# Kernel tuning notes

Hardware: AMD Instinct MI355X
Metric: run time of the kernel (lower is better)

## Reference

```python
import jax, jax.numpy as jnp
import numpy as np

B, T = 4, 1024
MF, EF, DM, DF, HN, L = 256, 512, 512, 2048, 8, 6
HD = DM // HN  # 64
D = MF + EF // 2  # 512, feature dim of x / mask_in


def prelu(x, a):
    return jnp.where(x >= 0, x, a * x)


def layer_norm(x, g, b, eps=1e-5):
    m = x.mean(-1, keepdims=True)
    v = ((x - m) ** 2).mean(-1, keepdims=True)
    return (x - m) / jnp.sqrt(v + eps) * g + b


def skew_relative(QE):
    # QE: (B, H, N, 2N-1) -> (B, H, N, N) via the pad/reshape/slice skew trick
    b, h, n = QE.shape[0], QE.shape[1], QE.shape[2]
    q = jnp.pad(QE, ((0, 0), (0, 0), (0, 0), (0, 1))).reshape(b, h, -1)
    q = jnp.pad(q, ((0, 0), (0, 0), (0, n - 1))).reshape(b, h, n + 1, 2 * n - 1)
    return q[:, :, :n, -n:]


def setup_inputs() -> dict:
    key = jax.random.key(0)
    ks = iter(jax.random.split(key, 80))
    rn = lambda shape, s: jax.random.normal(next(ks), shape, dtype=jnp.float32) * s
    si = lambda fan: fan ** -0.5
    inp = {}
    inp['x'] = rn((B, T, D), 1.0)
    inp['mask_in'] = (jax.random.uniform(next(ks), (B, T, D)) > 0.2).astype(jnp.float32)
    inp['p_kf'] = rn((B, T, 2), 1.0)
    inp['enc_w1'] = rn((2 * D, DM), si(2 * D)); inp['enc_b1'] = jnp.zeros((DM,)); inp['enc_a1'] = 0.25 * jnp.ones((1,))
    inp['enc_w2'] = rn((DM, DM), si(DM)); inp['enc_b2'] = jnp.zeros((DM,)); inp['enc_a2'] = 0.25 * jnp.ones((1,))
    inp['kf_w1'] = rn((2, DM), si(2)); inp['kf_b1'] = jnp.zeros((DM,)); inp['kf_a'] = 0.25 * jnp.ones((1,))
    inp['kf_w2'] = rn((DM, DM), si(DM)); inp['kf_b2'] = jnp.zeros((DM,))
    inp['rel_w1'] = rn((1, DM), 1.0); inp['rel_b1'] = jnp.zeros((DM,)); inp['rel_a'] = 0.25 * jnp.ones((1,))
    inp['rel_w2'] = rn((DM, HD), si(DM)); inp['rel_b2'] = jnp.zeros((HD,))
    inp['ln_g'] = jnp.ones((DM,)); inp['ln_b'] = jnp.zeros((DM,))
    inp['attn_wq'] = rn((L, DM, DM), si(DM))
    inp['attn_wk'] = rn((L, DM, DM), si(DM))
    inp['attn_wv'] = rn((L, DM, DM), si(DM))
    inp['attn_wo'] = rn((L, DM, DM), si(DM)); inp['attn_wob'] = jnp.zeros((L, DM))
    inp['ffn_w1'] = rn((L, DM, DF), si(DM)); inp['ffn_b1'] = jnp.zeros((L, DF)); inp['ffn_a'] = 0.25 * jnp.ones((L, 1))
    inp['ffn_w2'] = rn((L, DF, DM), si(DF)); inp['ffn_b2'] = jnp.zeros((L, DM))
    inp['dec_w1'] = rn((DM, DM), si(DM)); inp['dec_b1'] = jnp.zeros((DM,)); inp['dec_a'] = 0.25 * jnp.ones((1,))
    inp['dec_w2'] = rn((DM, MF), si(DM)); inp['dec_b2'] = jnp.zeros((MF,))
    return inp


def reference(x, mask_in, p_kf, enc_w1, enc_b1, enc_a1, enc_w2, enc_b2, enc_a2,
              kf_w1, kf_b1, kf_a, kf_w2, kf_b2, rel_w1, rel_b1, rel_a, rel_w2, rel_b2,
              ln_g, ln_b, attn_wq, attn_wk, attn_wv, attn_wo, attn_wob,
              ffn_w1, ffn_b1, ffn_a, ffn_w2, ffn_b2, dec_w1, dec_b1, dec_a, dec_w2, dec_b2):
    b, t, _ = x.shape
    # keyframe positional encoding + context encoder
    pe_kf = prelu(p_kf @ kf_w1 + kf_b1, kf_a) @ kf_w2 + kf_b2
    h = prelu(jnp.concatenate([x, mask_in], -1) @ enc_w1 + enc_b1, enc_a1)
    h = prelu(h @ enc_w2 + enc_b2, enc_a2) + pe_kf
    # relative position embedding table E: (2T-1, HD)
    rel = jnp.arange(-t + 1, t, dtype=jnp.float32)[:, None]
    E = prelu(rel @ rel_w1 + rel_b1, rel_a) @ rel_w2 + rel_b2
    # attention mask from mask_in (broadcast over heads/queries)
    valid = mask_in.sum(-1) > 0
    mask_att = jnp.where(valid, 0.0, -1e9)[:, None, None, :]  # (B,1,1,T)
    scale = HD ** -0.5
    nl = attn_wq.shape[0]
    for i in range(nl):
        hn = layer_norm(h, ln_g, ln_b)
        Q = (hn @ attn_wq[i]).reshape(b, t, HN, HD).transpose(0, 2, 1, 3)
        K = (hn @ attn_wk[i]).reshape(b, t, HN, HD).transpose(0, 2, 1, 3)
        V = (hn @ attn_wv[i]).reshape(b, t, HN, HD).transpose(0, 2, 1, 3)
        att = jnp.einsum('bhqd,bhkd->bhqk', Q, K)
        att = att + skew_relative(jnp.einsum('bhqd,rd->bhqr', Q, E))
        att = jax.nn.softmax(att * scale + mask_att, axis=-1)
        o = jnp.einsum('bhqk,bhkd->bhqd', att, V).transpose(0, 2, 1, 3).reshape(b, t, HN * HD)
        h = h + o @ attn_wo[i] + attn_wob[i]
        hn = layer_norm(h, ln_g, ln_b)
        h = h + prelu(hn @ ffn_w1[i] + ffn_b1[i], ffn_a[i]) @ ffn_w2[i] + ffn_b2[i]
    return prelu(h @ dec_w1 + dec_b1, dec_a) @ dec_w2 + dec_b2
```

## Files before the change

### kernel.cpp

```cpp
#include <hip/hip_runtime.h>
#include <cstddef>

#define BB 4
#define TT 1024
#define DMODEL 512
#define DFF 2048
#define NHEAD 8
#define HDIM 64
#define NTOK (BB*TT)
#define NLAYER 6
#define MFOUT 256
#define LDS_STRIDE 72
#define SPLITK 4

typedef __attribute__((ext_vector_type(8))) _Float16 f16x8;
typedef __attribute__((ext_vector_type(8))) short bf16x8;
typedef __attribute__((ext_vector_type(4))) float f32x4;
#define MFMAH(a,b,c) __builtin_amdgcn_mfma_f32_16x16x32_f16(a,b,c,0,0,0)
#define MFMAB(a,b,c) __builtin_amdgcn_mfma_f32_16x16x32_bf16(a,b,c,0,0,0)

union F16U { _Float16 h; unsigned short u; };

__device__ __forceinline__ unsigned f2bf(float f) {
    union { float f; unsigned u; } v; v.f = f;
    return (v.u + 0x7FFFu + ((v.u >> 16) & 1u)) >> 16;
}
__device__ __forceinline__ float bf2f(unsigned h) {
    union { unsigned u; float f; } v; v.u = h << 16;
    return v.f;
}
__device__ __forceinline__ unsigned short f16u(float v) {
    F16U t; t.h = (_Float16)v; return t.u;
}

#define MODE_F32  0
#define MODE_BF   1
#define MODE_QKV  5

__global__ __launch_bounds__(256)
void wcvt(const float* __restrict__ W, unsigned short* __restrict__ Wh,
          unsigned short* __restrict__ Wl, int N, int K)
{
    __shared__ unsigned short Hs[64][LDS_STRIDE];
    __shared__ unsigned short Ls[64][LDS_STRIDE];
    const int tid = threadIdx.x;
    const int n0 = blockIdx.x * 64, k0 = blockIdx.y * 64;
    #pragma unroll
    for (int i = 0; i < 4; i++) {
        const int idx = tid + i * 256;
        const int r = idx >> 4, c4 = (idx & 15) * 4;
        const float4 v = *(const float4*)&W[(size_t)(k0 + r) * N + n0 + c4];
        const float va[4] = {v.x, v.y, v.z, v.w};
        #pragma unroll
        for (int j = 0; j < 4; j++) {
            const unsigned h = f2bf(va[j]);
            Hs[c4 + j][r] = (unsigned short)h;
            Ls[c4 + j][r] = (unsigned short)f2bf(va[j] - bf2f(h));
        }
    }
    __syncthreads();
    #pragma unroll
    for (int i = 0; i < 2; i++) {
        const int idx = tid + i * 256;
        const int r = idx >> 3, c8 = (idx & 7) * 8;
        *(uint4*)&Wh[(size_t)(n0 + r) * K + k0 + c8] = *(const uint4*)&Hs[r][c8];
        *(uint4*)&Wl[(size_t)(n0 + r) * K + k0 + c8] = *(const uint4*)&Ls[r][c8];
    }
}

__global__ __launch_bounds__(256)
void gemm_l(const unsigned short* __restrict__ Ah, const unsigned short* __restrict__ Al,
            const unsigned short* __restrict__ Wh, const unsigned short* __restrict__ Wl,
            const float* __restrict__ bias, const float* __restrict__ alpha,
            const float* __restrict__ res, float* __restrict__ outf,
            unsigned short* __restrict__ o1, unsigned short* __restrict__ o2,
            unsigned short* __restrict__ o3, unsigned short* __restrict__ o4,
            unsigned short* __restrict__ o5, int N, int K, int mode)
{
    __shared__ __align__(16) unsigned short Ahs[64*LDS_STRIDE];
    __shared__ __align__(16) unsigned short Als[64*LDS_STRIDE];
    __shared__ __align__(16) unsigned short Whs[64*LDS_STRIDE];
    __shared__ __align__(16) unsigned short Wls[64*LDS_STRIDE];
    const int tid = threadIdx.x;
    const int lane = tid & 63, w = tid >> 6;
    const int wm = w >> 1, wn = w & 1;
    const int quad = lane >> 4, c = lane & 15;
    const int m0 = blockIdx.y * 64, n0 = blockIdx.x * 64;
    const int sr = tid >> 2, sc = (tid & 3) * 16;

    f32x4 acc[2][2];
    #pragma unroll
    for (int mi = 0; mi < 2; mi++)
        #pragma unroll
        for (int ni = 0; ni < 2; ni++) { acc[mi][ni][0]=0.f; acc[mi][ni][1]=0.f; acc[mi][ni][2]=0.f; acc[mi][ni][3]=0.f; }

    for (int k0 = 0; k0 < K; k0 += 64) {
        const size_t ga = (size_t)(m0 + sr) * K + k0 + sc;
        const size_t gb = (size_t)(n0 + sr) * K + k0 + sc;
        const int ls = sr * LDS_STRIDE + sc;
        *(uint4*)&Ahs[ls]     = *(const uint4*)&Ah[ga];
        *(uint4*)&Ahs[ls + 8] = *(const uint4*)&Ah[ga + 8];
        *(uint4*)&Als[ls]     = *(const uint4*)&Al[ga];
        *(uint4*)&Als[ls + 8] = *(const uint4*)&Al[ga + 8];
        *(uint4*)&Whs[ls]     = *(const uint4*)&Wh[gb];
        *(uint4*)&Whs[ls + 8] = *(const uint4*)&Wh[gb + 8];
        *(uint4*)&Wls[ls]     = *(const uint4*)&Wl[gb];
        *(uint4*)&Wls[ls + 8] = *(const uint4*)&Wl[gb + 8];
        __syncthreads();
        #pragma unroll
        for (int s = 0; s < 2; s++) {
            const int ao = (wm * 32 + c) * LDS_STRIDE + s * 32 + quad * 8;
            const int bo = (wn * 32 + c) * LDS_STRIDE + s * 32 + quad * 8;
            const bf16x8 ah0 = *(const bf16x8*)&Ahs[ao];
            const bf16x8 ah1 = *(const bf16x8*)&Ahs[ao + 16 * LDS_STRIDE];
            const bf16x8 al0 = *(const bf16x8*)&Als[ao];
            const bf16x8 al1 = *(const bf16x8*)&Als[ao + 16 * LDS_STRIDE];
            const bf16x8 bh0 = *(const bf16x8*)&Whs[bo];
            const bf16x8 bh1 = *(const bf16x8*)&Whs[bo + 16 * LDS_STRIDE];
            const bf16x8 bl0 = *(const bf16x8*)&Wls[bo];
            const bf16x8 bl1 = *(const bf16x8*)&Wls[bo + 16 * LDS_STRIDE];
            acc[0][0] = MFMAB(ah0, bh0, acc[0][0]);
            acc[0][1] = MFMAB(ah0, bh1, acc[0][1]);
            acc[1][0] = MFMAB(ah1, bh0, acc[1][0]);
            acc[1][1] = MFMAB(ah1, bh1, acc[1][1]);
            acc[0][0] = MFMAB(al0, bh0, acc[0][0]);
            acc[0][1] = MFMAB(al0, bh1, acc[0][1]);
            acc[1][0] = MFMAB(al1, bh0, acc[1][0]);
            acc[1][1] = MFMAB(al1, bh1, acc[1][1]);
            acc[0][0] = MFMAB(ah0, bl0, acc[0][0]);
            acc[0][1] = MFMAB(ah0, bl1, acc[0][1]);
            acc[1][0] = MFMAB(ah1, bl0, acc[1][0]);
            acc[1][1] = MFMAB(ah1, bl1, acc[1][1]);
        }
        __syncthreads();
    }
    const float alv = alpha ? alpha[0] : 0.f;
    #pragma unroll
    for (int mi = 0; mi < 2; mi++)
        #pragma unroll
        for (int ni = 0; ni < 2; ni++) {
            const int gn = n0 + wn * 32 + ni * 16 + c;
            const int gmb = m0 + wm * 32 + mi * 16 + quad * 4;
            const float bv = bias ? bias[gn] : 0.f;
            float v4[4];
            #pragma unroll
            for (int r = 0; r < 4; r++) {
                float v = acc[mi][ni][r] + bv;
                if (alpha) v = (v >= 0.f) ? v : alv * v;
                v4[r] = v;
            }
            if (mode == MODE_F32) {
                #pragma unroll
                for (int r = 0; r < 4; r++) {
                    const size_t oix = (size_t)(gmb + r) * N + gn;
                    outf[oix] = v4[r] + (res ? res[oix] : 0.f);
                }
            } else if (mode == MODE_BF) {
                #pragma unroll
                for (int r = 0; r < 4; r++) {
                    const size_t oix = (size_t)(gmb + r) * N + gn;
                    const unsigned h = f2bf(v4[r]);
                    o1[oix] = (unsigned short)h;
                    o2[oix] = (unsigned short)f2bf(v4[r] - bf2f(h));
                }
            } else {
                const int seg = gn >> 9;
                if (seg == 0) {
                    #pragma unroll
                    for (int r = 0; r < 4; r++) {
                        const size_t qix = (size_t)(gmb + r) * 512 + gn;
                        F16U t; t.h = (_Float16)v4[r];
                        o1[qix] = t.u;
                        o2[qix] = f16u((v4[r] - (float)t.h) * 1024.f);
                    }
                } else if (seg == 1) {
                    #pragma unroll
                    for (int r = 0; r < 4; r++)
                        o3[(size_t)(gmb + r) * 512 + (gn - 512)] = f16u(v4[r]);
                } else {
                    const int d512 = gn - 1024;
                    const int bbp = gmb >> 10, t0 = gmb & 1023;
                    const size_t vix = ((size_t)(bbp * 8 + (d512 >> 6)) * 64 + (d512 & 63)) * 1024 + t0;
                    ushort4 hv, lv;
                    unsigned short* hp = (unsigned short*)&hv;
                    unsigned short* lp = (unsigned short*)&lv;
                    #pragma unroll
                    for (int r = 0; r < 4; r++) {
                        F16U t; t.h = (_Float16)v4[r];
                        hp[r] = t.u;
                        lp[r] = f16u(v4[r] - (float)t.h);
                    }
                    *(ushort4*)&o4[vix] = hv;
                    *(ushort4*)&o5[vix] = lv;
                }
            }
        }
}

__global__ __launch_bounds__(64)
void ln_kernel(const float* __restrict__ x, const float* __restrict__ g,
               const float* __restrict__ b, unsigned short* __restrict__ oh,
               unsigned short* __restrict__ ol)
{
    const int token = blockIdx.x;
    const int lane = threadIdx.x;
    const float* row = x + (size_t)token * DMODEL;
    float v[8];
    *(float4*)&v[0] = *(const float4*)&row[lane * 4];
    *(float4*)&v[4] = *(const float4*)&row[256 + lane * 4];
    float s = 0.f, s2 = 0.f;
    #pragma unroll
    for (int i = 0; i < 8; i++) { s += v[i]; s2 += v[i] * v[i]; }
    #pragma unroll
    for (int off = 1; off < 64; off <<= 1) {
        s  += __shfl_xor(s, off);
        s2 += __shfl_xor(s2, off);
    }
    const float mean = s * (1.f / DMODEL);
    const float var  = s2 * (1.f / DMODEL) - mean * mean;
    const float rstd = rsqrtf(var + 1e-5f);
    #pragma unroll
    for (int hh = 0; hh < 2; hh++) {
        const int base = hh * 256 + lane * 4;
        const float4 gv = *(const float4*)&g[base];
        const float4 bv = *(const float4*)&b[base];
        float o[4];
        o[0] = (v[hh*4+0] - mean) * rstd * gv.x + bv.x;
        o[1] = (v[hh*4+1] - mean) * rstd * gv.y + bv.y;
        o[2] = (v[hh*4+2] - mean) * rstd * gv.z + bv.z;
        o[3] = (v[hh*4+3] - mean) * rstd * gv.w + bv.w;
        ushort4 ph, pl;
        unsigned short* php = (unsigned short*)&ph;
        unsigned short* plp = (unsigned short*)&pl;
        #pragma unroll
        for (int j = 0; j < 4; j++) {
            const unsigned hb = f2bf(o[j]);
            php[j] = (unsigned short)hb;
            plp[j] = (unsigned short)f2bf(o[j] - bf2f(hb));
        }
        *(ushort4*)&oh[(size_t)token * DMODEL + base] = ph;
        *(ushort4*)&ol[(size_t)token * DMODEL + base] = pl;
    }
}

__global__ __launch_bounds__(256)
void cvt_pair(const float* __restrict__ x, unsigned short* __restrict__ oh,
              unsigned short* __restrict__ ol)
{
    const int idx = (blockIdx.x * 256 + threadIdx.x) * 4;
    const float4 v = *(const float4*)&x[idx];
    const float va[4] = {v.x, v.y, v.z, v.w};
    ushort4 ph, pl;
    unsigned short* php = (unsigned short*)&ph;
    unsigned short* plp = (unsigned short*)&pl;
    #pragma unroll
    for (int j = 0; j < 4; j++) {
        const unsigned hb = f2bf(va[j]);
        php[j] = (unsigned short)hb;
        plp[j] = (unsigned short)f2bf(va[j] - bf2f(hb));
    }
    *(ushort4*)&oh[idx] = ph;
    *(ushort4*)&ol[idx] = pl;
}

__global__ __launch_bounds__(256)
void cvt_cat(const float* __restrict__ x, const float* __restrict__ mask,
             unsigned short* __restrict__ oh, unsigned short* __restrict__ ol)
{
    const int idx = (blockIdx.x * 256 + threadIdx.x) * 4;
    const int row = idx >> 10, col = idx & 1023;
    const float* src = (col < 512) ? &x[(size_t)row * 512 + col]
                                   : &mask[(size_t)row * 512 + col - 512];
    const float4 v = *(const float4*)src;
    const float va[4] = {v.x, v.y, v.z, v.w};
    ushort4 ph, pl;
    unsigned short* php = (unsigned short*)&ph;
    unsigned short* plp = (unsigned short*)&pl;
    #pragma unroll
    for (int j = 0; j < 4; j++) {
        const unsigned hb = f2bf(va[j]);
        php[j] = (unsigned short)hb;
        plp[j] = (unsigned short)f2bf(va[j] - bf2f(hb));
    }
    *(ushort4*)&oh[idx] = ph;
    *(ushort4*)&ol[idx] = pl;
}

__global__ __launch_bounds__(64)
void mask_kernel(const float* __restrict__ mask_in, float* __restrict__ mk)
{
    const int token = blockIdx.x;
    const int lane = threadIdx.x;
    const float* row = mask_in + (size_t)token * DMODEL;
    const float4 a = *(const float4*)&row[lane * 4];
    const float4 c = *(const float4*)&row[256 + lane * 4];
    float s = a.x + a.y + a.z + a.w + c.x + c.y + c.z + c.w;
    #pragma unroll
    for (int off = 1; off < 64; off <<= 1) s += __shfl_xor(s, off);
    if (lane == 0) mk[token] = (s > 0.f) ? 0.f : -1e9f;
}

__global__ __launch_bounds__(64)
void e_kernel(const float* __restrict__ w1, const float* __restrict__ b1,
              const float* __restrict__ a1, const float* __restrict__ w2,
              const float* __restrict__ b2,
              unsigned short* __restrict__ Ehi, unsigned short* __restrict__ Elo)
{
    __shared__ float t1[DMODEL];
    const int r = blockIdx.x;
    const int lane = threadIdx.x;
    const float rel = (float)r - 1023.f;
    const float al = a1[0];
    for (int j = lane; j < DMODEL; j += 64) {
        float v = rel * w1[j] + b1[j];
        t1[j] = (v >= 0.f) ? v : al * v;
    }
    __syncthreads();
    float acc = b2[lane];
    for (int j = 0; j < DMODEL; j++)
        acc = fmaf(t1[j], w2[j * HDIM + lane], acc);
    F16U t; t.h = (_Float16)acc;
    Ehi[(size_t)r * HDIM + lane] = t.u;
    Elo[(size_t)r * HDIM + lane] = f16u(acc - (float)t.h);
}

__global__ __launch_bounds__(256)
void kf1_kernel(const float* __restrict__ p, const float* __restrict__ w1,
                const float* __restrict__ b1, const float* __restrict__ a1,
                unsigned short* __restrict__ oh, unsigned short* __restrict__ ol)
{
    const int idx = blockIdx.x * 256 + threadIdx.x;
    const int m = idx >> 9, n = idx & 511;
    float v = fmaf(p[m*2], w1[n], fmaf(p[m*2+1], w1[DMODEL + n], b1[n]));
    v = (v >= 0.f) ? v : a1[0] * v;
    const unsigned hb = f2bf(v);
    oh[idx] = (unsigned short)hb;
    ol[idx] = (unsigned short)f2bf(v - bf2f(hb));
}

__global__ __launch_bounds__(256, 3)
void attn_mfma(const _Float16* __restrict__ qhg, const _Float16* __restrict__ qmg,
               const _Float16* __restrict__ kg, const _Float16* __restrict__ vth,
               const _Float16* __restrict__ vtl, const _Float16* __restrict__ Ehi,
               const _Float16* __restrict__ Elo, const float* __restrict__ mk,
               float* __restrict__ Opart, float* __restrict__ Mpart,
               float* __restrict__ Lpart)
{
    __shared__ __align__(16) _Float16 Ks [64*LDS_STRIDE];
    __shared__ __align__(16) _Float16 Vhs[64*LDS_STRIDE];
    __shared__ __align__(16) _Float16 Vls[64*LDS_STRIDE];
    __shared__ __align__(16) _Float16 Phs[64*LDS_STRIDE];
    __shared__ __align__(16) _Float16 Pls[64*LDS_STRIDE];

    const int tid = threadIdx.x;
    const int lane = tid & 63;
    const int w = tid >> 6;
    const int quad = lane >> 4;
    const int c = lane & 15;
    const int q0 = (blockIdx.x >> 2) * 64;
    const int split = blockIdx.x & 3;
    const int hh = blockIdx.y;
    const int bb = blockIdx.z;
    const size_t base = (size_t)bb * TT * DMODEL + (size_t)hh * HDIM;
    const size_t vbase = (size_t)(bb * NHEAD + hh) * HDIM * TT;
    const float* mkp = mk + bb * TT;
    const int srow = tid >> 3;
    const int scol = (tid & 7) * 8;

    f16x8 qh[2], qm[2];
    {
        const size_t qrow = base + (size_t)(q0 + 16 * w + c) * DMODEL;
        #pragma unroll
        for (int s = 0; s < 2; s++) {
            qh[s] = *(const f16x8*)&qhg[qrow + s * 32 + quad * 8];
            qm[s] = *(const f16x8*)&qmg[qrow + s * 32 + quad * 8];
        }
    }

    f32x4 O[4];
    #pragma unroll
    for (int dt = 0; dt < 4; dt++) { O[dt][0]=0.f; O[dt][1]=0.f; O[dt][2]=0.f; O[dt][3]=0.f; }
    float mrun[4] = {-1e30f, -1e30f, -1e30f, -1e30f};
    float lrun[4] = {0.f, 0.f, 0.f, 0.f};
    const int Jb = 48 - 16 * w;

    const int ktlo = split * (16 / SPLITK);
    for (int kt = ktlo; kt < ktlo + (16 / SPLITK); kt++) {
        const int k0 = kt * 64;
        const int rbase = k0 - q0 + 960;

        #pragma unroll
        for (int rr = 0; rr < 2; rr++) {
            const int row = srow + rr * 32;
            *(f16x8*)&Ks [row * LDS_STRIDE + scol] =
                *(const f16x8*)&kg [base + (size_t)(k0 + row) * DMODEL + scol];
            *(f16x8*)&Vhs[row * LDS_STRIDE + scol] =
                *(const f16x8*)&vth[vbase + (size_t)row * TT + k0 + scol];
            *(f16x8*)&Vls[row * LDS_STRIDE + scol] =
                *(const f16x8*)&vtl[vbase + (size_t)row * TT + k0 + scol];
        }
        __syncthreads();

        f32x4 S[4];
        #pragma unroll
        for (int t = 0; t < 4; t++) { S[t][0]=0.f; S[t][1]=0.f; S[t][2]=0.f; S[t][3]=0.f; }
        #pragma unroll
        for (int t = 0; t < 4; t++) {
            const int ko = (16 * t + c) * LDS_STRIDE + quad * 8;
            #pragma unroll
            for (int s = 0; s < 2; s++) {
                const f16x8 kf = *(const f16x8*)&Ks[ko + s * 32];
                S[t] = MFMAH(qh[s], kf, S[t]);
            }
        }
        f32x4 R[5], R2[5];
        #pragma unroll
        for (int u = 0; u < 5; u++) {
            R[u][0]=0.f; R[u][1]=0.f; R[u][2]=0.f; R[u][3]=0.f;
            R2[u][0]=0.f; R2[u][1]=0.f; R2[u][2]=0.f; R2[u][3]=0.f;
        }
        #pragma unroll
        for (int u = 0; u < 5; u++) {
            int gr = rbase + Jb + 16 * u + c;
            gr = gr < 0 ? 0 : (gr > 2046 ? 2046 : gr);
            const size_t eb = (size_t)gr * HDIM;
            const f16x8 eh0 = *(const f16x8*)&Ehi[eb + quad * 8];
            const f16x8 eh1 = *(const f16x8*)&Ehi[eb + 32 + quad * 8];
            const f16x8 el0 = *(const f16x8*)&Elo[eb + quad * 8];
            const f16x8 el1 = *(const f16x8*)&Elo[eb + 32 + quad * 8];
            R[u]  = MFMAH(qh[0], eh0, R[u]);
            R[u]  = MFMAH(qh[1], eh1, R[u]);
            R[u]  = MFMAH(qh[0], el0, R[u]);
            R[u]  = MFMAH(qh[1], el1, R[u]);
            R2[u] = MFMAH(qm[0], eh0, R2[u]);
            R2[u] = MFMAH(qm[1], eh1, R2[u]);
        }
        #pragma unroll
        for (int u = 0; u < 5; u++)
            #pragma unroll
            for (int r = 0; r < 4; r++)
                R[u][r] = fmaf(R2[u][r], 9.765625e-4f, R[u][r]);
        float bp[4][5];
        #pragma unroll
        for (int r = 0; r < 4; r++) {
            const int q = quad * 4 + r;
            const int srcl = (quad << 4) | ((c - q + 15) & 15);
            #pragma unroll
            for (int u = 0; u < 5; u++)
                bp[r][u] = __int_as_float(__builtin_amdgcn_ds_bpermute(srcl << 2, __float_as_int(R[u][r])));
        }
        float mkv[4];
        #pragma unroll
        for (int t = 0; t < 4; t++) mkv[t] = mkp[k0 + 16*t + c];
        float tmax[4] = {-3e38f, -3e38f, -3e38f, -3e38f};
        #pragma unroll
        for (int t = 0; t < 4; t++)
            #pragma unroll
            for (int r = 0; r < 4; r++) {
                const int q = quad*4 + r;
                const int jj = 16*t + c - q + 15;
                const float rv = ((jj >> 4) == t) ? bp[r][t] : bp[r][t+1];
                const float v = (S[t][r] + rv) * 0.125f + mkv[t];
                S[t][r] = v;
                tmax[r] = fmaxf(tmax[r], v);
            }
        #pragma unroll
        for (int r = 0; r < 4; r++) {
            tmax[r] = fmaxf(tmax[r], __shfl_xor(tmax[r], 1));
            tmax[r] = fmaxf(tmax[r], __shfl_xor(tmax[r], 2));
            tmax[r] = fmaxf(tmax[r], __shfl_xor(tmax[r], 4));
            tmax[r] = fmaxf(tmax[r], __shfl_xor(tmax[r], 8));
        }
        float corr[4];
        #pragma unroll
        for (int r = 0; r < 4; r++) {
            const float mn = fmaxf(mrun[r], tmax[r]);
            corr[r] = __expf(mrun[r] - mn);
            mrun[r] = mn;
            lrun[r] *= corr[r];
        }
        #pragma unroll
        for (int dt = 0; dt < 4; dt++)
            #pragma unroll
            for (int r = 0; r < 4; r++) O[dt][r] *= corr[r];
        float psum[4] = {0.f, 0.f, 0.f, 0.f};
        #pragma unroll
        for (int t = 0; t < 4; t++)
            #pragma unroll
            for (int r = 0; r < 4; r++) {
                const float p = __expf(S[t][r] - mrun[r]);
                psum[r] += p;
                const _Float16 hp = (_Float16)p;
                Phs[(w*16 + quad*4 + r)*LDS_STRIDE + 16*t + c] = hp;
                Pls[(w*16 + quad*4 + r)*LDS_STRIDE + 16*t + c] = (_Float16)(p - (float)hp);
            }
        #pragma unroll
        for (int r = 0; r < 4; r++) {
            psum[r] += __shfl_xor(psum[r], 1);
            psum[r] += __shfl_xor(psum[r], 2);
            psum[r] += __shfl_xor(psum[r], 4);
            psum[r] += __shfl_xor(psum[r], 8);
            lrun[r] += psum[r];
        }
        f16x8 pfh[2], pfl[2];
        #pragma unroll
        for (int s = 0; s < 2; s++) {
            pfh[s] = *(const f16x8*)&Phs[(w*16 + c)*LDS_STRIDE + s*32 + quad*8];
            pfl[s] = *(const f16x8*)&Pls[(w*16 + c)*LDS_STRIDE + s*32 + quad*8];
        }
        #pragma unroll
        for (int dt = 0; dt < 4; dt++) {
            const int vo = (16 * dt + c) * LDS_STRIDE + quad * 8;
            #pragma unroll
            for (int s = 0; s < 2; s++) {
                const f16x8 vhf = *(const f16x8*)&Vhs[vo + s * 32];
                const f16x8 vlf = *(const f16x8*)&Vls[vo + s * 32];
                O[dt] = MFMAH(pfh[s], vhf, O[dt]);
                O[dt] = MFMAH(pfl[s], vhf, O[dt]);
                O[dt] = MFMAH(pfh[s], vlf, O[dt]);
            }
        }
        __syncthreads();
    }
    const size_t obase = (size_t)((split * BB + bb) * NHEAD + hh) * TT + q0 + 16 * w;
    #pragma unroll
    for (int r = 0; r < 4; r++) {
        if (c == 0) {
            Mpart[obase + quad * 4 + r] = mrun[r];
            Lpart[obase + quad * 4 + r] = lrun[r];
        }
    }
    #pragma unroll
    for (int dt = 0; dt < 4; dt++)
        #pragma unroll
        for (int r = 0; r < 4; r++)
            Opart[(obase + quad * 4 + r) * HDIM + 16 * dt + c] = O[dt][r];
}

__global__ __launch_bounds__(256)
void attn_combine(const float* __restrict__ Opart, const float* __restrict__ Mpart,
                  const float* __restrict__ Lpart,
                  unsigned short* __restrict__ obh, unsigned short* __restrict__ obl)
{
    const int tid = threadIdx.x;
    const int row = blockIdx.x * 16 + (tid >> 4);
    const int d0 = (tid & 15) * 4;
    const int SR = BB * NHEAD * TT;
    float mv[SPLITK];
    float m = -3e38f;
    #pragma unroll
    for (int i = 0; i < SPLITK; i++) { mv[i] = Mpart[i * SR + row]; m = fmaxf(m, mv[i]); }
    float wv[SPLITK];
    float l = 0.f;
    #pragma unroll
    for (int i = 0; i < SPLITK; i++) {
        wv[i] = __expf(mv[i] - m);
        l += wv[i] * Lpart[i * SR + row];
    }
    const float inv = 1.f / l;
    float o[4] = {0.f, 0.f, 0.f, 0.f};
    #pragma unroll
    for (int i = 0; i < SPLITK; i++) {
        const float4 v = *(const float4*)&Opart[((size_t)i * SR + row) * HDIM + d0];
        o[0] = fmaf(wv[i], v.x, o[0]);
        o[1] = fmaf(wv[i], v.y, o[1]);
        o[2] = fmaf(wv[i], v.z, o[2]);
        o[3] = fmaf(wv[i], v.w, o[3]);
    }
    const int q = row & (TT - 1), bh = row >> 10;
    const size_t oix = ((size_t)((bh >> 3) * TT + q)) * DMODEL + (size_t)(bh & 7) * HDIM + d0;
    ushort4 ph, pl;
    unsigned short* php = (unsigned short*)&ph;
    unsigned short* plp = (unsigned short*)&pl;
    #pragma unroll
    for (int j = 0; j < 4; j++) {
        const float v = o[j] * inv;
        const unsigned hb = f2bf(v);
        php[j] = (unsigned short)hb;
        plp[j] = (unsigned short)f2bf(v - bf2f(hb));
    }
    *(ushort4*)&obh[oix] = ph;
    *(ushort4*)&obl[oix] = pl;
}

extern "C" void kernel_launch(void* const* d_in, const int* in_sizes, int n_in,
                              void* d_out, int out_size, void* d_ws, size_t ws_size,
                              hipStream_t stream)
{
    const float* x       = (const float*)d_in[0];
    const float* mask_in = (const float*)d_in[1];
    const float* p_kf    = (const float*)d_in[2];
    const float* enc_w1  = (const float*)d_in[3];
    const float* enc_b1  = (const float*)d_in[4];
    const float* enc_a1  = (const float*)d_in[5];
    const float* enc_w2  = (const float*)d_in[6];
    const float* enc_b2  = (const float*)d_in[7];
    const float* enc_a2  = (const float*)d_in[8];
    const float* kf_w1   = (const float*)d_in[9];
    const float* kf_b1   = (const float*)d_in[10];
    const float* kf_a    = (const float*)d_in[11];
    const float* kf_w2   = (const float*)d_in[12];
    const float* kf_b2   = (const float*)d_in[13];
    const float* rel_w1  = (const float*)d_in[14];
    const float* rel_b1  = (const float*)d_in[15];
    const float* rel_a   = (const float*)d_in[16];
    const float* rel_w2  = (const float*)d_in[17];
    const float* rel_b2  = (const float*)d_in[18];
    const float* ln_g    = (const float*)d_in[19];
    const float* ln_b    = (const float*)d_in[20];
    const float* wq      = (const float*)d_in[21];
    const float* wk      = (const float*)d_in[22];
    const float* wv      = (const float*)d_in[23];
    const float* wo      = (const float*)d_in[24];
    const float* wob     = (const float*)d_in[25];
    const float* fw1     = (const float*)d_in[26];
    const float* fb1     = (const float*)d_in[27];
    const float* fa      = (const float*)d_in[28];
    const float* fw2     = (const float*)d_in[29];
    const float* fb2     = (const float*)d_in[30];
    const float* dw1     = (const float*)d_in[31];
    const float* db1     = (const float*)d_in[32];
    const float* da      = (const float*)d_in[33];
    const float* dw2     = (const float*)d_in[34];
    const float* db2     = (const float*)d_in[35];
    float* out = (float*)d_out;

    char* p = (char*)d_ws;
    const size_t SZ_TD  = (size_t)NTOK * DMODEL;
    float* h = (float*)p;                 p += SZ_TD * 4;
    unsigned short* hnh = (unsigned short*)p; p += SZ_TD * 2;
    unsigned short* hnl = (unsigned short*)p; p += SZ_TD * 2;
    unsigned short* qhg = (unsigned short*)p; p += SZ_TD * 2;
    unsigned short* qmg = (unsigned short*)p; p += SZ_TD * 2;
    unsigned short* kg  = (unsigned short*)p; p += SZ_TD * 2;
    unsigned short* vhg = (unsigned short*)p; p += SZ_TD * 2;
    unsigned short* vlg = (unsigned short*)p; p += SZ_TD * 2;
    unsigned short* obh = (unsigned short*)p; p += SZ_TD * 2;
    unsigned short* obl = (unsigned short*)p; p += SZ_TD * 2;
    unsigned short* midh = (unsigned short*)p; p += (size_t)NTOK * DFF * 2;
    unsigned short* midl = (unsigned short*)p; p += (size_t)NTOK * DFF * 2;
    unsigned short* Ehi = (unsigned short*)p; p += (size_t)2048 * HDIM * 2;
    unsigned short* Elo = (unsigned short*)p; p += (size_t)2048 * HDIM * 2;
    float* mk = (float*)p;                p += (size_t)NTOK * 4;
    unsigned short* qkvh = (unsigned short*)p; p += (size_t)1536 * 512 * 2;
    unsigned short* qkvl = (unsigned short*)p; p += (size_t)1536 * 512 * 2;
    unsigned short* woh  = (unsigned short*)p; p += (size_t)512 * 512 * 2;
    unsigned short* wol  = (unsigned short*)p; p += (size_t)512 * 512 * 2;
    unsigned short* f1h  = (unsigned short*)p; p += (size_t)2048 * 512 * 2;
    unsigned short* f1l  = (unsigned short*)p; p += (size_t)2048 * 512 * 2;
    unsigned short* f2h  = (unsigned short*)p; p += (size_t)512 * 2048 * 2;
    unsigned short* f2l  = (unsigned short*)p; p += (size_t)512 * 2048 * 2;
    float* pe = (float*)obh;
    float* Opart = (float*)midh;
    float* Mpart = (float*)hnh;
    float* Lpart = Mpart + (size_t)SPLITK * BB * NHEAD * TT;

    const dim3 blk256(256), blk64(64);
    const dim3 gN512(8, 64);
    const dim3 gQKV(24, 64);
    const dim3 gFFN1(32, 64);
    const dim3 gN256(4, 64);
    #define NP nullptr

    e_kernel<<<dim3(2047), blk64, 0, stream>>>(rel_w1, rel_b1, rel_a, rel_w2, rel_b2, Ehi, Elo);
    mask_kernel<<<dim3(NTOK), blk64, 0, stream>>>(mask_in, mk);
    wcvt<<<dim3(8, 8), blk256, 0, stream>>>(kf_w2, woh, wol, 512, 512);
    wcvt<<<dim3(8, 16), blk256, 0, stream>>>(enc_w1, f1h, f1l, 512, 1024);
    wcvt<<<dim3(8, 8), blk256, 0, stream>>>(enc_w2, qkvh, qkvl, 512, 512);
    kf1_kernel<<<dim3(NTOK*DMODEL/256), blk256, 0, stream>>>(p_kf, kf_w1, kf_b1, kf_a, qhg, qmg);
    gemm_l<<<gN512, blk256, 0, stream>>>(qhg, qmg, woh, wol, kf_b2, NP, NP, pe,
                                         NP, NP, NP, NP, NP, DMODEL, DMODEL, MODE_F32);
    cvt_cat<<<dim3(NTOK*1024/1024), blk256, 0, stream>>>(x, mask_in, midh, midl);
    gemm_l<<<gN512, blk256, 0, stream>>>(midh, midl, f1h, f1l, enc_b1, enc_a1, NP, NP,
                                         hnh, hnl, NP, NP, NP, DMODEL, 2*DMODEL, MODE_BF);
    gemm_l<<<gN512, blk256, 0, stream>>>(hnh, hnl, qkvh, qkvl, enc_b2, enc_a2, pe, h,
                                         NP, NP, NP, NP, NP, DMODEL, DMODEL, MODE_F32);

    for (int i = 0; i < NLAYER; i++) {
        const size_t wofs = (size_t)i * DMODEL * DMODEL;
        wcvt<<<dim3(8, 8), blk256, 0, stream>>>(wq + wofs, qkvh, qkvl, 512, 512);
        wcvt<<<dim3(8, 8), blk256, 0, stream>>>(wk + wofs, qkvh + 512*512, qkvl + 512*512, 512, 512);
        wcvt<<<dim3(8, 8), blk256, 0, stream>>>(wv + wofs, qkvh + 1024*512, qkvl + 1024*512, 512, 512);
        wcvt<<<dim3(8, 8), blk256, 0, stream>>>(wo + wofs, woh, wol, 512, 512);
        wcvt<<<dim3(32, 8), blk256, 0, stream>>>(fw1 + (size_t)i*DMODEL*DFF, f1h, f1l, 2048, 512);
        wcvt<<<dim3(8, 32), blk256, 0, stream>>>(fw2 + (size_t)i*DFF*DMODEL, f2h, f2l, 512, 2048);

        ln_kernel<<<dim3(NTOK), blk64, 0, stream>>>(h, ln_g, ln_b, hnh, hnl);
        gemm_l<<<gQKV, blk256, 0, stream>>>(hnh, hnl, qkvh, qkvl, NP, NP, NP, NP,
                                            qhg, qmg, kg, vhg, vlg, 1536, DMODEL, MODE_QKV);
        attn_mfma<<<dim3((TT/64)*SPLITK, NHEAD, BB), blk256, 0, stream>>>(
            (const _Float16*)qhg, (const _Float16*)qmg, (const _Float16*)kg,
            (const _Float16*)vhg, (const _Float16*)vlg,
            (const _Float16*)Ehi, (const _Float16*)Elo, mk, Opart, Mpart, Lpart);
        attn_combine<<<dim3(BB*NHEAD*TT/16), blk256, 0, stream>>>(Opart, Mpart, Lpart, obh, obl);
        gemm_l<<<gN512, blk256, 0, stream>>>(obh, obl, woh, wol, wob + (size_t)i*DMODEL,
                                             NP, h, h, NP, NP, NP, NP, NP, DMODEL, DMODEL, MODE_F32);
        ln_kernel<<<dim3(NTOK), blk64, 0, stream>>>(h, ln_g, ln_b, hnh, hnl);
        gemm_l<<<gFFN1, blk256, 0, stream>>>(hnh, hnl, f1h, f1l, fb1 + (size_t)i*DFF, fa + i,
                                             NP, NP, midh, midl, NP, NP, NP, DFF, DMODEL, MODE_BF);
        gemm_l<<<gN512, blk256, 0, stream>>>(midh, midl, f2h, f2l, fb2 + (size_t)i*DMODEL,
                                             NP, h, h, NP, NP, NP, NP, NP, DMODEL, DFF, MODE_F32);
    }
    wcvt<<<dim3(8, 8), blk256, 0, stream>>>(dw1, woh, wol, 512, 512);
    wcvt<<<dim3(4, 8), blk256, 0, stream>>>(dw2, f2h, f2l, 256, 512);
    cvt_pair<<<dim3(SZ_TD/1024), blk256, 0, stream>>>(h, hnh, hnl);
    gemm_l<<<gN512, blk256, 0, stream>>>(hnh, hnl, woh, wol, db1, da, NP, NP,
                                         midh, midl, NP, NP, NP, DMODEL, DMODEL, MODE_BF);
    gemm_l<<<gN256, blk256, 0, stream>>>(midh, midl, f2h, f2l, db2, NP, NP, out,
                                         NP, NP, NP, NP, NP, MFOUT, DMODEL, MODE_F32);
    #undef NP
}
```

Baseline: 1.977 ms.

## Widen attention blocks to 128 queries, prefetch K/V, pre-swizzle E table

The attention kernel now runs 512-thread blocks covering 128 query rows. Each K/V tile staged in LDS is therefore shared by twice as many waves, and the P buffers grow to match. The next K/V tile is prefetched into registers while the current one is computed on, which aims to hide global latency behind the MFMA work. The relative-position table E is written in MFMA fragment order with one padded row, so each lane reads a contiguous vector without clamping or address arithmetic. In exchange, LDS use and register pressure rise and there are fewer blocks per head, and the kernel's wave-offset logic (Jb) must hold for eight waves.

```diff
diff --git a/kernel.cpp b/kernel.cpp
--- a/kernel.cpp
+++ b/kernel.cpp
@@ -308,8 +308,9 @@
 {
     __shared__ float t1[DMODEL];
     const int r = blockIdx.x;
+    const int rr = (r > 2046) ? 2046 : r;
     const int lane = threadIdx.x;
-    const float rel = (float)r - 1023.f;
+    const float rel = (float)rr - 1023.f;
     const float al = a1[0];
     for (int j = lane; j < DMODEL; j += 64) {
         float v = rel * w1[j] + b1[j];
@@ -319,9 +320,13 @@
     float acc = b2[lane];
     for (int j = 0; j < DMODEL; j++)
         acc = fmaf(t1[j], w2[j * HDIM + lane], acc);
+    const int g = r >> 4, s = lane >> 5;
+    const int l = (((lane >> 3) & 3) << 4) | (r & 15);
+    const int j = lane & 7;
+    const size_t adr = ((size_t)(g * 2 + s) * 64 + l) * 8 + j;
     F16U t; t.h = (_Float16)acc;
-    Ehi[(size_t)r * HDIM + lane] = t.u;
-    Elo[(size_t)r * HDIM + lane] = f16u(acc - (float)t.h);
+    Ehi[adr] = t.u;
+    Elo[adr] = f16u(acc - (float)t.h);
 }
 
 __global__ __launch_bounds__(256)
@@ -338,7 +343,7 @@
     ol[idx] = (unsigned short)f2bf(v - bf2f(hb));
 }
 
-__global__ __launch_bounds__(256, 3)
+__global__ __launch_bounds__(512, 4)
 void attn_mfma(const _Float16* __restrict__ qhg, const _Float16* __restrict__ qmg,
                const _Float16* __restrict__ kg, const _Float16* __restrict__ vth,
                const _Float16* __restrict__ vtl, const _Float16* __restrict__ Ehi,
@@ -349,15 +354,15 @@
     __shared__ __align__(16) _Float16 Ks [64*LDS_STRIDE];
     __shared__ __align__(16) _Float16 Vhs[64*LDS_STRIDE];
     __shared__ __align__(16) _Float16 Vls[64*LDS_STRIDE];
-    __shared__ __align__(16) _Float16 Phs[64*LDS_STRIDE];
-    __shared__ __align__(16) _Float16 Pls[64*LDS_STRIDE];
+    __shared__ __align__(16) _Float16 Phs[128*LDS_STRIDE];
+    __shared__ __align__(16) _Float16 Pls[128*LDS_STRIDE];
 
     const int tid = threadIdx.x;
     const int lane = tid & 63;
     const int w = tid >> 6;
     const int quad = lane >> 4;
     const int c = lane & 15;
-    const int q0 = (blockIdx.x >> 2) * 64;
+    const int q0 = (blockIdx.x >> 2) * 128;
     const int split = blockIdx.x & 3;
     const int hh = blockIdx.y;
     const int bb = blockIdx.z;
@@ -385,21 +390,28 @@
     const int Jb = 48 - 16 * w;
 
     const int ktlo = split * (16 / SPLITK);
+    f16x8 sk, svh, svl;
+    {
+        const int k0 = ktlo * 64;
+        sk  = *(const f16x8*)&kg [base + (size_t)(k0 + srow) * DMODEL + scol];
+        svh = *(const f16x8*)&vth[vbase + (size_t)srow * TT + k0 + scol];
+        svl = *(const f16x8*)&vtl[vbase + (size_t)srow * TT + k0 + scol];
+    }
     for (int kt = ktlo; kt < ktlo + (16 / SPLITK); kt++) {
         const int k0 = kt * 64;
         const int rbase = k0 - q0 + 960;
 
-        #pragma unroll
-        for (int rr = 0; rr < 2; rr++) {
-            const int row = srow + rr * 32;
-            *(f16x8*)&Ks [row * LDS_STRIDE + scol] =
-                *(const f16x8*)&kg [base + (size_t)(k0 + row) * DMODEL + scol];
-            *(f16x8*)&Vhs[row * LDS_STRIDE + scol] =
-                *(const f16x8*)&vth[vbase + (size_t)row * TT + k0 + scol];
-            *(f16x8*)&Vls[row * LDS_STRIDE + scol] =
-                *(const f16x8*)&vtl[vbase + (size_t)row * TT + k0 + scol];
-        }
+        *(f16x8*)&Ks [srow * LDS_STRIDE + scol] = sk;
+        *(f16x8*)&Vhs[srow * LDS_STRIDE + scol] = svh;
+        *(f16x8*)&Vls[srow * LDS_STRIDE + scol] = svl;
         __syncthreads();
+        {
+            const int kn = (kt + 1 < 16) ? (kt + 1) : kt;
+            const int k0n = kn * 64;
+            sk  = *(const f16x8*)&kg [base + (size_t)(k0n + srow) * DMODEL + scol];
+            svh = *(const f16x8*)&vth[vbase + (size_t)srow * TT + k0n + scol];
+            svl = *(const f16x8*)&vtl[vbase + (size_t)srow * TT + k0n + scol];
+        }
 
         f32x4 S[4];
         #pragma unroll
@@ -421,13 +433,13 @@
         }
         #pragma unroll
         for (int u = 0; u < 5; u++) {
-            int gr = rbase + Jb + 16 * u + c;
-            gr = gr < 0 ? 0 : (gr > 2046 ? 2046 : gr);
-            const size_t eb = (size_t)gr * HDIM;
-            const f16x8 eh0 = *(const f16x8*)&Ehi[eb + quad * 8];
-            const f16x8 eh1 = *(const f16x8*)&Ehi[eb + 32 + quad * 8];
-            const f16x8 el0 = *(const f16x8*)&Elo[eb + quad * 8];
-            const f16x8 el1 = *(const f16x8*)&Elo[eb + 32 + quad * 8];
+            const int g = (rbase + Jb + 16 * u) >> 4;
+            const size_t eb0 = ((size_t)(g * 2 + 0) * 64 + lane) * 8;
+            const size_t eb1 = ((size_t)(g * 2 + 1) * 64 + lane) * 8;
+            const f16x8 eh0 = *(const f16x8*)&Ehi[eb0];
+            const f16x8 eh1 = *(const f16x8*)&Ehi[eb1];
+            const f16x8 el0 = *(const f16x8*)&Elo[eb0];
+            const f16x8 el1 = *(const f16x8*)&Elo[eb1];
             R[u]  = MFMAH(qh[0], eh0, R[u]);
             R[u]  = MFMAH(qh[1], eh1, R[u]);
             R[u]  = MFMAH(qh[0], el0, R[u]);
@@ -655,14 +667,14 @@
     float* Mpart = (float*)hnh;
     float* Lpart = Mpart + (size_t)SPLITK * BB * NHEAD * TT;
 
-    const dim3 blk256(256), blk64(64);
+    const dim3 blk256(256), blk64(64), blk512(512);
     const dim3 gN512(8, 64);
     const dim3 gQKV(24, 64);
     const dim3 gFFN1(32, 64);
     const dim3 gN256(4, 64);
     #define NP nullptr
 
-    e_kernel<<<dim3(2047), blk64, 0, stream>>>(rel_w1, rel_b1, rel_a, rel_w2, rel_b2, Ehi, Elo);
+    e_kernel<<<dim3(2048), blk64, 0, stream>>>(rel_w1, rel_b1, rel_a, rel_w2, rel_b2, Ehi, Elo);
     mask_kernel<<<dim3(NTOK), blk64, 0, stream>>>(mask_in, mk);
     wcvt<<<dim3(8, 8), blk256, 0, stream>>>(kf_w2, woh, wol, 512, 512);
     wcvt<<<dim3(8, 16), blk256, 0, stream>>>(enc_w1, f1h, f1l, 512, 1024);
@@ -688,7 +700,7 @@
         ln_kernel<<<dim3(NTOK), blk64, 0, stream>>>(h, ln_g, ln_b, hnh, hnl);
         gemm_l<<<gQKV, blk256, 0, stream>>>(hnh, hnl, qkvh, qkvl, NP, NP, NP, NP,
                                             qhg, qmg, kg, vhg, vlg, 1536, DMODEL, MODE_QKV);
-        attn_mfma<<<dim3((TT/64)*SPLITK, NHEAD, BB), blk256, 0, stream>>>(
+        attn_mfma<<<dim3((TT/128)*SPLITK, NHEAD, BB), blk512, 0, stream>>>(
             (const _Float16*)qhg, (const _Float16*)qmg, (const _Float16*)kg,
             (const _Float16*)vhg, (const _Float16*)vlg,
             (const _Float16*)Ehi, (const _Float16*)Elo, mk, Opart, Mpart, Lpart);
```

Result: faster. 1.916 ms (-3.1%).
